# Performance work log

Measured on AMD Instinct MI355X. Metric: run time of the kernel, lower is better.

Reference implementation:

```python
import jax, jax.numpy as jnp
import numpy as np

N = 50000


def gcn_conv(x, edge_index, W, b):
    # x: [N, F_in], edge_index: [2, E] (row=source j, col=target i)
    n = x.shape[0]
    loops = jnp.arange(n, dtype=edge_index.dtype)
    row = jnp.concatenate([edge_index[0], loops])
    col = jnp.concatenate([edge_index[1], loops])
    # linear transform first (PyG GCNConv)
    xw = x @ W  # [N, F_out]
    # symmetric normalization deg^{-1/2}[row] * deg^{-1/2}[col]
    deg = jax.ops.segment_sum(jnp.ones_like(col, dtype=xw.dtype), col, num_segments=n)
    dis = jnp.where(deg > 0, jax.lax.rsqrt(jnp.maximum(deg, 1e-12)), 0.0)
    norm = dis[row] * dis[col]  # [E+N]
    # gather-scale-scatter: sum_j norm_ij * (W x_j)
    msgs = xw[row] * norm[:, None]
    out = jax.ops.segment_sum(msgs, col, num_segments=n)
    return out + b


def setup_inputs() -> dict:
    key = jax.random.key(0)
    k1, k2, k3, k4, k5 = jax.random.split(key, 5)
    in_dim, hidden_dim, out_dim = 128, 128, 64
    x = jax.random.normal(k1, (N, in_dim), dtype=jnp.float32)
    edge_index = jax.random.randint(k2, (2, 800000), 0, N, dtype=jnp.int64)
    s1 = 1.0 / np.sqrt(in_dim)
    s2 = 1.0 / np.sqrt(hidden_dim)
    W1 = jax.random.uniform(k3, (in_dim, hidden_dim), jnp.float32, -s1, s1)
    b1 = jnp.zeros((hidden_dim,), jnp.float32)
    W2 = jax.random.uniform(k4, (hidden_dim, out_dim), jnp.float32, -s2, s2)
    b2 = jnp.zeros((out_dim,), jnp.float32)
    return {"x": x, "edge_index": edge_index, "W1": W1, "b1": b1, "W2": W2, "b2": b2}


def reference(x, edge_index, W1, b1, W2, b2):
    h = gcn_conv(x, edge_index, W1, b1)
    h = jax.nn.relu(h)
    # dropout(p=0.5, training=False) -> identity (inference reference)
    out = gcn_conv(h, edge_index, W2, b2)
    return out
```

## Files before the change

kernel.cpp:

```cpp
#include <hip/hip_runtime.h>
#include <hip/hip_fp16.h>


typedef _Float16 half8 __attribute__((ext_vector_type(8)));
typedef float floatx4 __attribute__((ext_vector_type(4)));

__global__ void k_count(const int* __restrict__ col, int* __restrict__ deg,
                        int* __restrict__ rank, int E) {
    int e = blockIdx.x * blockDim.x + threadIdx.x;
    if (e < E) rank[e] = atomicAdd(&deg[col[e]], 1);
}

__global__ __launch_bounds__(1024) void k_scan_local(const int* __restrict__ deg,
                                                     int* __restrict__ rowptr,
                                                     int* __restrict__ praw,
                                                     int* __restrict__ bsum,
                                                     float* __restrict__ dis, int n) {
    __shared__ int wsum[16];
    int b = blockIdx.x, tid = threadIdx.x;
    int lane = tid & 63, w = tid >> 6;
    int i = b * 1024 + tid;
    int v = (i < n) ? deg[i] : 0;
    if (i < n) dis[i] = rsqrtf((float)v + 1.0f);
    int sc = v;
#pragma unroll
    for (int off = 1; off < 64; off <<= 1) {
        int t = __shfl_up(sc, off);
        if (lane >= off) sc += t;
    }
    if (lane == 63) wsum[w] = sc;
    __syncthreads();
    if (w == 0) {
        int s = (lane < 16) ? wsum[lane] : 0;
#pragma unroll
        for (int off = 1; off < 16; off <<= 1) {
            int t = __shfl_up(s, off);
            if (lane >= off) s += t;
        }
        if (lane < 16) wsum[lane] = s;
    }
    __syncthreads();
    int incl = sc + ((w > 0) ? wsum[w - 1] : 0);
    if (i < n) {
        rowptr[i + 1] = incl;
        praw[i + 1] = incl;
    }
    if (tid == 1023) bsum[b] = incl;
    if (b == 0 && tid == 0) {
        rowptr[0] = 0;
        praw[0] = 0;
    }
}

template <int N, typename AT>
__device__ __forceinline__ void gemm_tile(const AT* __restrict__ X,
                                          const float* __restrict__ W,
                                          const float* __restrict__ scale,
                                          __half* __restrict__ Y, int M,
                                          int m0, __half2* wt, int tid) {
    for (int i = tid; i < N * 64; i += 256) {
        int nn = i & (N - 1);
        int k2 = i / N;
        float w0 = W[(size_t)(2 * k2) * N + nn];
        float w1 = W[(size_t)(2 * k2 + 1) * N + nn];
        wt[nn * 64 + ((k2 >> 2) ^ (nn & 15)) * 4 + (k2 & 3)] = __floats2half2_rn(w0, w1);
    }
    __syncthreads();
    int wid = tid >> 6, lane = tid & 63;
    int col = lane & 15, quad = lane >> 4;
    int m_a = m0 + wid * 16 + col;
    bool a_ok = m_a < M;
    constexpr int NT = N / 16;
    floatx4 acc[NT] = {};
#pragma unroll
    for (int ks = 0; ks < 4; ++ks) {
        int k = ks * 32 + quad * 8;
        half8 af;
        if constexpr (sizeof(AT) == 4) {
            floatx4 a0 = {0.f, 0.f, 0.f, 0.f}, a1 = {0.f, 0.f, 0.f, 0.f};
            if (a_ok) {
                a0 = *(const floatx4*)&X[(size_t)m_a * 128 + k];
                a1 = *(const floatx4*)&X[(size_t)m_a * 128 + k + 4];
            }
            af = half8{(_Float16)a0[0], (_Float16)a0[1], (_Float16)a0[2], (_Float16)a0[3],
                       (_Float16)a1[0], (_Float16)a1[1], (_Float16)a1[2], (_Float16)a1[3]};
        } else {
            half8 t = {};
            if (a_ok) t = *(const half8*)(const void*)&X[(size_t)m_a * 128 + k];
            af = t;
        }
        int kblk = ks * 4 + quad;
#pragma unroll
        for (int nt = 0; nt < NT; ++nt) {
            int nn = nt * 16 + col;
            half8 bf = *(const half8*)(const void*)&wt[nn * 64 + (kblk ^ (nn & 15)) * 4];
            acc[nt] = __builtin_amdgcn_mfma_f32_16x16x32_f16(af, bf, acc[nt], 0, 0, 0);
        }
    }
    int mbase = m0 + wid * 16 + quad * 4;
    float s[4];
#pragma unroll
    for (int r = 0; r < 4; ++r) s[r] = (mbase + r < M) ? scale[mbase + r] : 0.f;
#pragma unroll
    for (int nt = 0; nt < NT; ++nt) {
#pragma unroll
        for (int r = 0; r < 4; ++r) {
            if (mbase + r < M)
                Y[(size_t)(mbase + r) * N + nt * 16 + col] = __float2half(acc[nt][r] * s[r]);
        }
    }
}

__global__ __launch_bounds__(256) void k_fused(int* __restrict__ rowptr,
                                               const int* __restrict__ bsum, int n,
                                               const float* __restrict__ X,
                                               const float* __restrict__ W,
                                               const float* __restrict__ scale,
                                               __half* __restrict__ Y, int M,
                                               int FB, int GB,
                                               const int* __restrict__ praw,
                                               const int* __restrict__ row,
                                               const int* __restrict__ col,
                                               const int* __restrict__ rank,
                                               int* __restrict__ csr, int E) {
    __shared__ __align__(16) __half2 wt[128 * 64];
    int b = blockIdx.x, tid = threadIdx.x;
    if (b < FB) {
        int* red = (int*)wt;
        int partial = 0;
        for (int j = tid; j < b; j += 256) partial += bsum[j];
        red[tid] = partial;
        __syncthreads();
        for (int off = 128; off > 0; off >>= 1) {
            if (tid < off) red[tid] += red[tid + off];
            __syncthreads();
        }
        int offv = red[0];
        if (offv == 0) return;
#pragma unroll
        for (int r = 0; r < 4; ++r) {
            int i = b * 1024 + r * 256 + tid;
            if (i < n) rowptr[i + 1] += offv;
        }
        return;
    }
    if (b >= FB + GB) {
        int* q = (int*)wt;
        int nb = (n + 1023) >> 10;
        if (tid < 64) {
            int v = (tid >= 1 && tid <= nb) ? bsum[tid - 1] : 0;
#pragma unroll
            for (int off = 1; off < 64; off <<= 1) {
                int t = __shfl_up(v, off);
                if ((tid & 63) >= off) v += t;
            }
            q[tid] = v;
        }
        __syncthreads();
        int base = (b - FB - GB) * 1024;
#pragma unroll
        for (int r = 0; r < 4; ++r) {
            int e = base + r * 256 + tid;
            if (e < E) {
                int c = col[e];
                int qi = (c == 0) ? 0 : ((c - 1) >> 10);
                csr[praw[c] + q[qi] + rank[e]] = row[e];
            }
        }
        return;
    }
    gemm_tile<128, float>(X, W, scale, Y, M, (b - FB) * 64, wt, tid);
}

__global__ __launch_bounds__(256) void k_agg_gemm(const __half* __restrict__ xw,
                                                  const float* __restrict__ dis,
                                                  const int* __restrict__ rowptr,
                                                  const int* __restrict__ csr,
                                                  const float* __restrict__ bias,
                                                  const float* __restrict__ W2,
                                                  __half* __restrict__ Y,
                                                  int n) {
    __shared__ __align__(16) half8 htile[64 * 16];
    __shared__ __align__(16) __half2 wt[64 * 64];
    int tid = threadIdx.x, b = blockIdx.x;
    int lane = tid & 63, w = tid >> 6;
    int q = lane >> 4, li = lane & 15;
    int qbase = lane & 48;

    for (int i = tid; i < 64 * 64; i += 256) {
        int nn = i & 63;
        int k2 = i >> 6;
        float w0 = W2[(size_t)(2 * k2) * 64 + nn];
        float w1 = W2[(size_t)(2 * k2 + 1) * 64 + nn];
        wt[nn * 64 + ((k2 >> 2) ^ (nn & 15)) * 4 + (k2 & 3)] = __floats2half2_rn(w0, w1);
    }

    const half8* rows = (const half8*)xw;
    floatx4 bb0 = *(const floatx4*)&bias[li * 8];
    floatx4 bb1 = *(const floatx4*)&bias[li * 8 + 4];

#pragma unroll
    for (int g = 0; g < 4; ++g) {
        int m_loc = g * 16 + (w << 2) + q;
        int node = b * 64 + m_loc;
        bool ok = node < n;
        float di = 0.f;
        int beg = 0, end = 0;
        if (ok) {
            di = dis[node];
            beg = rowptr[node];
            end = rowptr[node + 1];
        }
        int dg = end - beg;
        int m1 = max(dg, __shfl(dg, lane ^ 16));
        int mx = max(m1, __shfl(m1, lane ^ 32));
        float acc[8] = {};
        if (ok) {
            half8 sf = rows[(size_t)node * 16 + li];
#pragma unroll
            for (int f = 0; f < 8; ++f) acc[f] = (float)sf[f];
        }
        int ecur = beg + (li & 7);
        int curidx = (0 < mx && ecur < end) ? csr[ecur] : 0;
        for (int i = 0; i < mx; i += 8) {
            int enx = beg + i + 8 + (li & 7);
            int nidx = (i + 8 < mx && enx < end) ? csr[enx] : 0;
            half8 v[8];
#pragma unroll
            for (int j = 0; j < 8; ++j) {
                int s = __shfl(curidx, qbase + j);
                v[j] = rows[(size_t)s * 16 + li];
            }
#pragma unroll
            for (int j = 0; j < 8; ++j) {
                if (beg + i + j < end) {
#pragma unroll
                    for (int f = 0; f < 8; ++f) acc[f] += (float)v[j][f];
                }
            }
            curidx = nidx;
        }
        half8 o = {};
        if (ok) {
#pragma unroll
            for (int f = 0; f < 4; ++f) o[f] = (_Float16)fmaxf(acc[f] * di + bb0[f], 0.f);
#pragma unroll
            for (int f = 0; f < 4; ++f) o[4 + f] = (_Float16)fmaxf(acc[4 + f] * di + bb1[f], 0.f);
        }
        htile[m_loc * 16 + (li ^ (m_loc & 7))] = o;
    }
    __syncthreads();

    int col16 = lane & 15, quad = lane >> 4;
    int m_loc = w * 16 + col16;
    floatx4 gacc[4] = {};
#pragma unroll
    for (int ks = 0; ks < 4; ++ks) {
        half8 af = htile[m_loc * 16 + ((ks * 4 + quad) ^ (m_loc & 7))];
        int kblk = ks * 4 + quad;
#pragma unroll
        for (int nt = 0; nt < 4; ++nt) {
            int nn = nt * 16 + col16;
            half8 bf = *(const half8*)(const void*)&wt[nn * 64 + (kblk ^ (nn & 15)) * 4];
            gacc[nt] = __builtin_amdgcn_mfma_f32_16x16x32_f16(af, bf, gacc[nt], 0, 0, 0);
        }
    }
    int mbase = b * 64 + w * 16 + quad * 4;
    float s[4];
#pragma unroll
    for (int r = 0; r < 4; ++r) s[r] = (mbase + r < n) ? dis[mbase + r] : 0.f;
#pragma unroll
    for (int nt = 0; nt < 4; ++nt) {
#pragma unroll
        for (int r = 0; r < 4; ++r) {
            if (mbase + r < n)
                Y[(size_t)(mbase + r) * 64 + nt * 16 + col16] = __float2half(gacc[nt][r] * s[r]);
        }
    }
}

__global__ __launch_bounds__(256) void k_agg64(const __half* __restrict__ xw,
                                               const float* __restrict__ dis,
                                               const int* __restrict__ rowptr,
                                               const int* __restrict__ csr,
                                               const float* __restrict__ bias,
                                               float* __restrict__ out, int n) {
    int tid = threadIdx.x;
    int lane = tid & 63;
    int o8 = lane >> 3, li = lane & 7;
    int obase = lane & 56;
    int node = blockIdx.x * 32 + ((tid >> 6) << 3) + o8;
    bool ok = node < n;
    float di = 0.f;
    int beg = 0, end = 0;
    if (ok) {
        di = dis[node];
        beg = rowptr[node];
        end = rowptr[node + 1];
    }
    int dg = end - beg;
    int m1 = max(dg, __shfl(dg, lane ^ 8));
    int m2 = max(m1, __shfl(m1, lane ^ 16));
    int mx = max(m2, __shfl(m2, lane ^ 32));
    const half8* rows = (const half8*)xw;
    float acc[8] = {};
    if (ok) {
        half8 sf = rows[(size_t)node * 8 + li];
#pragma unroll
        for (int f = 0; f < 8; ++f) acc[f] = (float)sf[f];
    }
    int ecur = beg + li;
    int curidx = (0 < mx && ecur < end) ? csr[ecur] : 0;
    for (int i = 0; i < mx; i += 8) {
        int enx = beg + i + 8 + li;
        int nidx = (i + 8 < mx && enx < end) ? csr[enx] : 0;
        half8 v[8];
#pragma unroll
        for (int j = 0; j < 8; ++j) {
            int s = __shfl(curidx, obase + j);
            v[j] = rows[(size_t)s * 8 + li];
        }
#pragma unroll
        for (int j = 0; j < 8; ++j) {
            if (beg + i + j < end) {
#pragma unroll
                for (int f = 0; f < 8; ++f) acc[f] += (float)v[j][f];
            }
        }
        curidx = nidx;
    }
    if (ok) {
        floatx4 b0 = *(const floatx4*)&bias[li * 8];
        floatx4 b1 = *(const floatx4*)&bias[li * 8 + 4];
        floatx4 o0, o1;
#pragma unroll
        for (int f = 0; f < 4; ++f) o0[f] = acc[f] * di + b0[f];
#pragma unroll
        for (int f = 0; f < 4; ++f) o1[f] = acc[4 + f] * di + b1[f];
        *(floatx4*)&out[(size_t)node * 64 + li * 8] = o0;
        *(floatx4*)&out[(size_t)node * 64 + li * 8 + 4] = o1;
    }
}

extern "C" void kernel_launch(void* const* d_in, const int* in_sizes, int n_in,
                              void* d_out, int out_size, void* d_ws, size_t ws_size,
                              hipStream_t stream) {
    const float* x  = (const float*)d_in[0];
    const int*   ei = (const int*)d_in[1];
    const float* W1 = (const float*)d_in[2];
    const float* b1 = (const float*)d_in[3];
    const float* W2 = (const float*)d_in[4];
    const float* b2 = (const float*)d_in[5];
    float* out = (float*)d_out;

    const int n = in_sizes[0] / 128;
    const int E = in_sizes[1] / 2;
    const int* row = ei;
    const int* col = ei + E;
    const int NB = (n + 1023) / 1024;
    const int CB = (E + 255) / 256;
    const int GB = (n + 63) / 64;
    const int FILLB = (E + 1023) / 1024;

    char* ws = (char*)d_ws;
    size_t off = 0;
    auto alloc = [&](size_t bytes) -> void* {
        void* p = ws + off;
        off += (bytes + 255) & ~(size_t)255;
        return p;
    };
    int*    deg    = (int*)alloc((size_t)n * 4);
    int*    rowptr = (int*)alloc((size_t)(n + 1) * 4);
    int*    praw   = (int*)alloc((size_t)(n + 1) * 4);
    int*    bsum   = (int*)alloc((size_t)NB * 4);
    int*    rank   = (int*)alloc((size_t)E * 4);
    int*    csr    = (int*)alloc((size_t)E * 4);
    float*  dis    = (float*)alloc((size_t)n * 4);
    __half* xw1    = (__half*)alloc((size_t)n * 128 * 2);
    __half* xw2    = (__half*)alloc((size_t)n * 64 * 2);
    (void)ws_size;

    hipMemsetAsync(deg, 0, (size_t)n * 4, stream);
    k_count<<<CB, 256, 0, stream>>>(col, deg, rank, E);
    k_scan_local<<<NB, 1024, 0, stream>>>(deg, rowptr, praw, bsum, dis, n);
    k_fused<<<NB + GB + FILLB, 256, 0, stream>>>(rowptr, bsum, n, x, W1, dis, xw1,
                                                 n, NB, GB, praw, row, col, rank,
                                                 csr, E);
    k_agg_gemm<<<GB, 256, 0, stream>>>(xw1, dis, rowptr, csr, b1, W2, xw2, n);
    k_agg64<<<(n + 31) / 32, 256, 0, stream>>>(xw2, dis, rowptr, csr, b2, out, n);
}
```

Measured before the change: 200.7 us.

## Split layer-1 GEMM into column halves, precast W2 once, reorder fused blocks

The layer-1 GEMM in the fused kernel now runs as two blocks per 64-row tile, each computing 64 output columns. This halves the shared memory and accumulators per block, which should allow more resident blocks. The CSR fill blocks now come before the rowptr-fix and GEMM blocks, so the latency-bound scatter starts first. W2 is converted once to a transposed fp16 buffer by an extra block in the scan kernel, and the aggregation kernel reads its B fragments from global memory instead of rebuilding a shared-memory copy in every block, with a launch-bounds occupancy hint added. The cost is that each X tile is read and converted twice, and the W2 fragments now come through global or cache loads.

```diff
diff --git a/kernel.cpp b/kernel.cpp
--- a/kernel.cpp
+++ b/kernel.cpp
@@ -15,9 +15,18 @@
                                                      int* __restrict__ rowptr,
                                                      int* __restrict__ praw,
                                                      int* __restrict__ bsum,
-                                                     float* __restrict__ dis, int n) {
+                                                     float* __restrict__ dis, int n,
+                                                     const float* __restrict__ W2,
+                                                     __half* __restrict__ w2h) {
     __shared__ int wsum[16];
     int b = blockIdx.x, tid = threadIdx.x;
+    if (b == gridDim.x - 1) {
+        for (int i = tid; i < 64 * 128; i += 1024) {
+            int nn = i >> 7, k = i & 127;
+            w2h[i] = __float2half(W2[(size_t)k * 64 + nn]);
+        }
+        return;
+    }
     int lane = tid & 63, w = tid >> 6;
     int i = b * 1024 + tid;
     int v = (i < n) ? deg[i] : 0;
@@ -52,17 +61,16 @@
     }
 }
 
-template <int N, typename AT>
-__device__ __forceinline__ void gemm_tile(const AT* __restrict__ X,
-                                          const float* __restrict__ W,
-                                          const float* __restrict__ scale,
-                                          __half* __restrict__ Y, int M,
-                                          int m0, __half2* wt, int tid) {
-    for (int i = tid; i < N * 64; i += 256) {
-        int nn = i & (N - 1);
-        int k2 = i / N;
-        float w0 = W[(size_t)(2 * k2) * N + nn];
-        float w1 = W[(size_t)(2 * k2 + 1) * N + nn];
+__device__ __forceinline__ void gemm1_half(const float* __restrict__ X,
+                                           const float* __restrict__ W1,
+                                           const float* __restrict__ scale,
+                                           __half* __restrict__ Y, int M,
+                                           int m0, int nh, __half2* wt, int tid) {
+    for (int i = tid; i < 64 * 64; i += 256) {
+        int nn = i & 63;
+        int k2 = i >> 6;
+        float w0 = W1[(size_t)(2 * k2) * 128 + nh * 64 + nn];
+        float w1 = W1[(size_t)(2 * k2 + 1) * 128 + nh * 64 + nn];
         wt[nn * 64 + ((k2 >> 2) ^ (nn & 15)) * 4 + (k2 & 3)] = __floats2half2_rn(w0, w1);
     }
     __syncthreads();
@@ -70,28 +78,20 @@
     int col = lane & 15, quad = lane >> 4;
     int m_a = m0 + wid * 16 + col;
     bool a_ok = m_a < M;
-    constexpr int NT = N / 16;
-    floatx4 acc[NT] = {};
+    floatx4 acc[4] = {};
 #pragma unroll
     for (int ks = 0; ks < 4; ++ks) {
         int k = ks * 32 + quad * 8;
-        half8 af;
-        if constexpr (sizeof(AT) == 4) {
-            floatx4 a0 = {0.f, 0.f, 0.f, 0.f}, a1 = {0.f, 0.f, 0.f, 0.f};
-            if (a_ok) {
-                a0 = *(const floatx4*)&X[(size_t)m_a * 128 + k];
-                a1 = *(const floatx4*)&X[(size_t)m_a * 128 + k + 4];
-            }
-            af = half8{(_Float16)a0[0], (_Float16)a0[1], (_Float16)a0[2], (_Float16)a0[3],
-                       (_Float16)a1[0], (_Float16)a1[1], (_Float16)a1[2], (_Float16)a1[3]};
-        } else {
-            half8 t = {};
-            if (a_ok) t = *(const half8*)(const void*)&X[(size_t)m_a * 128 + k];
-            af = t;
-        }
+        floatx4 a0 = {0.f, 0.f, 0.f, 0.f}, a1 = {0.f, 0.f, 0.f, 0.f};
+        if (a_ok) {
+            a0 = *(const floatx4*)&X[(size_t)m_a * 128 + k];
+            a1 = *(const floatx4*)&X[(size_t)m_a * 128 + k + 4];
+        }
+        half8 af = half8{(_Float16)a0[0], (_Float16)a0[1], (_Float16)a0[2], (_Float16)a0[3],
+                         (_Float16)a1[0], (_Float16)a1[1], (_Float16)a1[2], (_Float16)a1[3]};
         int kblk = ks * 4 + quad;
 #pragma unroll
-        for (int nt = 0; nt < NT; ++nt) {
+        for (int nt = 0; nt < 4; ++nt) {
             int nn = nt * 16 + col;
             half8 bf = *(const half8*)(const void*)&wt[nn * 64 + (kblk ^ (nn & 15)) * 4];
             acc[nt] = __builtin_amdgcn_mfma_f32_16x16x32_f16(af, bf, acc[nt], 0, 0, 0);
@@ -102,11 +102,12 @@
 #pragma unroll
     for (int r = 0; r < 4; ++r) s[r] = (mbase + r < M) ? scale[mbase + r] : 0.f;
 #pragma unroll
-    for (int nt = 0; nt < NT; ++nt) {
+    for (int nt = 0; nt < 4; ++nt) {
 #pragma unroll
         for (int r = 0; r < 4; ++r) {
             if (mbase + r < M)
-                Y[(size_t)(mbase + r) * N + nt * 16 + col] = __float2half(acc[nt][r] * s[r]);
+                Y[(size_t)(mbase + r) * 128 + nh * 64 + nt * 16 + col] =
+                    __float2half(acc[nt][r] * s[r]);
         }
     }
 }
@@ -114,37 +115,18 @@
 __global__ __launch_bounds__(256) void k_fused(int* __restrict__ rowptr,
                                                const int* __restrict__ bsum, int n,
                                                const float* __restrict__ X,
-                                               const float* __restrict__ W,
+                                               const float* __restrict__ W1,
                                                const float* __restrict__ scale,
                                                __half* __restrict__ Y, int M,
-                                               int FB, int GB,
+                                               int FB, int FILLB,
                                                const int* __restrict__ praw,
                                                const int* __restrict__ row,
                                                const int* __restrict__ col,
                                                const int* __restrict__ rank,
                                                int* __restrict__ csr, int E) {
-    __shared__ __align__(16) __half2 wt[128 * 64];
+    __shared__ __align__(16) __half2 wt[64 * 64];
     int b = blockIdx.x, tid = threadIdx.x;
-    if (b < FB) {
-        int* red = (int*)wt;
-        int partial = 0;
-        for (int j = tid; j < b; j += 256) partial += bsum[j];
-        red[tid] = partial;
-        __syncthreads();
-        for (int off = 128; off > 0; off >>= 1) {
-            if (tid < off) red[tid] += red[tid + off];
-            __syncthreads();
-        }
-        int offv = red[0];
-        if (offv == 0) return;
-#pragma unroll
-        for (int r = 0; r < 4; ++r) {
-            int i = b * 1024 + r * 256 + tid;
-            if (i < n) rowptr[i + 1] += offv;
-        }
-        return;
-    }
-    if (b >= FB + GB) {
+    if (b < FILLB) {
         int* q = (int*)wt;
         int nb = (n + 1023) >> 10;
         if (tid < 64) {
@@ -157,7 +139,7 @@
             q[tid] = v;
         }
         __syncthreads();
-        int base = (b - FB - GB) * 1024;
+        int base = b * 1024;
 #pragma unroll
         for (int r = 0; r < 4; ++r) {
             int e = base + r * 256 + tid;
@@ -169,31 +151,43 @@
         }
         return;
     }
-    gemm_tile<128, float>(X, W, scale, Y, M, (b - FB) * 64, wt, tid);
-}
-
-__global__ __launch_bounds__(256) void k_agg_gemm(const __half* __restrict__ xw,
-                                                  const float* __restrict__ dis,
-                                                  const int* __restrict__ rowptr,
-                                                  const int* __restrict__ csr,
-                                                  const float* __restrict__ bias,
-                                                  const float* __restrict__ W2,
-                                                  __half* __restrict__ Y,
-                                                  int n) {
+    if (b < FILLB + FB) {
+        int bb = b - FILLB;
+        int* red = (int*)wt;
+        int partial = 0;
+        for (int j = tid; j < bb; j += 256) partial += bsum[j];
+        red[tid] = partial;
+        __syncthreads();
+        for (int off = 128; off > 0; off >>= 1) {
+            if (tid < off) red[tid] += red[tid + off];
+            __syncthreads();
+        }
+        int offv = red[0];
+        if (offv == 0) return;
+#pragma unroll
+        for (int r = 0; r < 4; ++r) {
+            int i = bb * 1024 + r * 256 + tid;
+            if (i < n) rowptr[i + 1] += offv;
+        }
+        return;
+    }
+    int gb = b - FILLB - FB;
+    gemm1_half(X, W1, scale, Y, M, (gb >> 1) * 64, gb & 1, wt, tid);
+}
+
+__global__ __launch_bounds__(256, 6) void k_agg_gemm(const __half* __restrict__ xw,
+                                                     const float* __restrict__ dis,
+                                                     const int* __restrict__ rowptr,
+                                                     const int* __restrict__ csr,
+                                                     const float* __restrict__ bias,
+                                                     const __half* __restrict__ w2h,
+                                                     __half* __restrict__ Y,
+                                                     int n) {
     __shared__ __align__(16) half8 htile[64 * 16];
-    __shared__ __align__(16) __half2 wt[64 * 64];
     int tid = threadIdx.x, b = blockIdx.x;
     int lane = tid & 63, w = tid >> 6;
     int q = lane >> 4, li = lane & 15;
     int qbase = lane & 48;
-
-    for (int i = tid; i < 64 * 64; i += 256) {
-        int nn = i & 63;
-        int k2 = i >> 6;
-        float w0 = W2[(size_t)(2 * k2) * 64 + nn];
-        float w1 = W2[(size_t)(2 * k2 + 1) * 64 + nn];
-        wt[nn * 64 + ((k2 >> 2) ^ (nn & 15)) * 4 + (k2 & 3)] = __floats2half2_rn(w0, w1);
-    }
 
     const half8* rows = (const half8*)xw;
     floatx4 bb0 = *(const floatx4*)&bias[li * 8];
@@ -261,7 +255,7 @@
 #pragma unroll
         for (int nt = 0; nt < 4; ++nt) {
             int nn = nt * 16 + col16;
-            half8 bf = *(const half8*)(const void*)&wt[nn * 64 + (kblk ^ (nn & 15)) * 4];
+            half8 bf = *(const half8*)(const void*)&w2h[nn * 128 + kblk * 8];
             gacc[nt] = __builtin_amdgcn_mfma_f32_16x16x32_f16(af, bf, gacc[nt], 0, 0, 0);
         }
     }
@@ -378,14 +372,15 @@
     float*  dis    = (float*)alloc((size_t)n * 4);
     __half* xw1    = (__half*)alloc((size_t)n * 128 * 2);
     __half* xw2    = (__half*)alloc((size_t)n * 64 * 2);
+    __half* w2h    = (__half*)alloc((size_t)64 * 128 * 2);
     (void)ws_size;
 
     hipMemsetAsync(deg, 0, (size_t)n * 4, stream);
     k_count<<<CB, 256, 0, stream>>>(col, deg, rank, E);
-    k_scan_local<<<NB, 1024, 0, stream>>>(deg, rowptr, praw, bsum, dis, n);
-    k_fused<<<NB + GB + FILLB, 256, 0, stream>>>(rowptr, bsum, n, x, W1, dis, xw1,
-                                                 n, NB, GB, praw, row, col, rank,
-                                                 csr, E);
-    k_agg_gemm<<<GB, 256, 0, stream>>>(xw1, dis, rowptr, csr, b1, W2, xw2, n);
+    k_scan_local<<<NB + 1, 1024, 0, stream>>>(deg, rowptr, praw, bsum, dis, n, W2, w2h);
+    k_fused<<<FILLB + NB + 2 * GB, 256, 0, stream>>>(rowptr, bsum, n, x, W1, dis, xw1,
+                                                     n, NB, FILLB, praw, row, col, rank,
+                                                     csr, E);
+    k_agg_gemm<<<GB, 256, 0, stream>>>(xw1, dis, rowptr, csr, b1, w2h, xw2, n);
     k_agg64<<<(n + 31) / 32, 256, 0, stream>>>(xw2, dis, rowptr, csr, b2, out, n);
 }
```

Measured after the change: 200.8 us. No clear change (+0.1%).
